# Performance work log

Hardware: AMD Instinct MI355X
Metric: run time of the kernel (lower is better)

The kernel has to match this reference:

```python
import jax, jax.numpy as jnp
import numpy as np

L, H, DK, DV, D, DH, V, S, B = 2, 12, 64, 64, 768, 3072, 32000, 1024, 2


def _layernorm(x):
    # matches custom LayerNorm: mean over last dim, biased std, no eps, no affine
    mu = jnp.mean(x, axis=-1, keepdims=True)
    sigma = jnp.sqrt(jnp.mean(jnp.square(x - mu), axis=-1, keepdims=True))
    return (x - mu) / sigma


def setup_inputs() -> dict:
    key = jax.random.key(0)
    ks = jax.random.split(key, 12)
    n = lambda k, shp: (0.02 * jax.random.normal(k, shp, dtype=jnp.float32))
    return {
        "x": jax.random.randint(ks[0], (B, S), 0, V),
        "ignore": jax.random.randint(ks[1], (B, S), 0, 2).astype(jnp.int32),
        "emb": n(ks[2], (V, D)),
        "pos": n(ks[3], (S, D)),
        "Wq": n(ks[4], (L, H, D, DK)), "bq": jnp.zeros((L, H, DK), jnp.float32),
        "Wk": n(ks[5], (L, H, D, DK)), "bk": jnp.zeros((L, H, DK), jnp.float32),
        "Wv": n(ks[6], (L, H, D, DV)), "bv": jnp.zeros((L, H, DV), jnp.float32),
        "Wo": n(ks[7], (L, H * DV, D)), "bo": jnp.zeros((L, D), jnp.float32),
        "W1": n(ks[8], (L, D, DH)), "b1": jnp.zeros((L, DH), jnp.float32),
        "W2": n(ks[9], (L, DH, D)), "b2": jnp.zeros((L, D), jnp.float32),
        "Wout": n(ks[10], (D, V)), "bout": jnp.zeros((V,), jnp.float32),
    }


def reference(x, ignore, emb, pos, Wq, bq, Wk, bk, Wv, bv, Wo, bo, W1, b1, W2, b2, Wout, bout):
    b, s = x.shape
    ign0 = (ignore == 0)  # True = valid token
    # token emb + position emb zeroed on ignored positions (dropout = eval/identity)
    h = emb[x] + pos[None, :, :] * ign0[:, :, None].astype(emb.dtype)

    # mask[b,i,j]: attend iff j<=i AND (ignore[j]==0 OR i==j)  (diagonal always kept)
    causal = jnp.tril(jnp.ones((s, s), dtype=bool))
    eye = jnp.eye(s, dtype=bool)
    allow = (ign0[:, None, None, :] | eye[None, None, :, :]) & causal[None, None, :, :]  # [b,1,i,j]

    scale = jnp.sqrt(jnp.asarray(DK, h.dtype))
    for l in range(L):
        q = jnp.einsum('bsd,hdk->bhsk', h, Wq[l]) + bq[l][None, :, None, :]
        k = jnp.einsum('bsd,hdk->bhsk', h, Wk[l]) + bk[l][None, :, None, :]
        v = jnp.einsum('bsd,hdv->bhsv', h, Wv[l]) + bv[l][None, :, None, :]
        scores = jnp.einsum('bhik,bhjk->bhij', q, k) / scale
        scores = jnp.where(allow, scores, -jnp.inf)
        p = jax.nn.softmax(scores, axis=-1)
        sa = jnp.einsum('bhij,bhjv->bhiv', p, v)
        sa = sa.transpose(0, 2, 1, 3).reshape(b, s, H * DV)  # concat heads (head-major order matches torch cat)
        attn_out = sa @ Wo[l] + bo[l]
        z = _layernorm(h + attn_out)
        # NOTE: original FeedForwardLayer applies GELU AFTER linear2 (faithful to source)
        f = jax.nn.gelu((z @ W1[l] + b1[l]) @ W2[l] + b2[l], approximate=False)
        h = _layernorm(z + f)
    return h @ Wout + bout
```

## Files before the change

### kernel.cpp

```cpp
#include <hip/hip_runtime.h>
#include <math.h>

static constexpr int L_ = 2, H_ = 12, D_ = 768, DH_ = 3072, V_ = 32000,
                     S_ = 1024, B_ = 2;
static constexpr int M_ = B_ * S_;

typedef __attribute__((ext_vector_type(4))) float f32x4;
typedef __attribute__((ext_vector_type(8))) short s16x8;
typedef __attribute__((ext_vector_type(2))) unsigned int u32x2;
typedef __attribute__((ext_vector_type(4))) unsigned int u32x4;

__device__ __forceinline__ unsigned short f2bf(float f) {
    unsigned u = __builtin_bit_cast(unsigned, f);
    u = (u + 0x7FFFu + ((u >> 16) & 1u)) >> 16;
    return (unsigned short)u;
}
__device__ __forceinline__ unsigned pack2(float a, float b) {
    return (unsigned)f2bf(a) | ((unsigned)f2bf(b) << 16);
}

__device__ __forceinline__ void gld16(const void* g, void* l) {
    __builtin_amdgcn_global_load_lds(
        (const __attribute__((address_space(1))) unsigned int*)g,
        (__attribute__((address_space(3))) unsigned int*)l, 16, 0, 0);
}

__global__ __launch_bounds__(256) void wtr_kernel(
    const float* __restrict__ in, unsigned short* __restrict__ out, int K, int N)
{
    __shared__ unsigned short t[64 * 68];
    const size_t mo = (size_t)blockIdx.z * K * N;
    in  += mo; out += mo;
    const int n0 = blockIdx.x * 64, k0 = blockIdx.y * 64;
    const int tid = threadIdx.x;
    const int kr = tid >> 2, nc = (tid & 3) * 16;
    const float* src = in + (size_t)(k0 + kr) * N + n0 + nc;
    #pragma unroll
    for (int j = 0; j < 4; ++j) {
        const float4 v = *(const float4*)(src + j * 4);
        *(u32x2*)&t[kr * 68 + nc + j * 4] = (u32x2){pack2(v.x, v.y), pack2(v.z, v.w)};
    }
    __syncthreads();
    const int nr = tid >> 2, kc = (tid & 3) * 16;
    unsigned short v16[16];
    #pragma unroll
    for (int j = 0; j < 16; ++j) v16[j] = t[(kc + j) * 68 + nr];
    unsigned short* dst = out + (size_t)(n0 + nr) * K + k0 + kc;
    ((u32x4*)dst)[0] = *(u32x4*)&v16[0];
    ((u32x4*)dst)[1] = *(u32x4*)&v16[8];
}

__global__ __launch_bounds__(256) void wtr3_kernel(
    const float* __restrict__ Wq, const float* __restrict__ Wk,
    const float* __restrict__ Wv, unsigned short* __restrict__ oq,
    unsigned short* __restrict__ ok, unsigned short* __restrict__ ov)
{
    __shared__ unsigned short t[64 * 68];
    const int z = blockIdx.z;
    const int which = z / 24, zz = z - which * 24;
    const float* in = (which == 0) ? Wq : (which == 1) ? Wk : Wv;
    unsigned short* out = (which == 0) ? oq : (which == 1) ? ok : ov;
    const size_t mo = (size_t)zz * D_ * 64;
    in += mo; out += mo;
    const int k0 = blockIdx.y * 64;
    const int tid = threadIdx.x;
    const int kr = tid >> 2, nc = (tid & 3) * 16;
    const float* src = in + (size_t)(k0 + kr) * 64 + nc;
    #pragma unroll
    for (int j = 0; j < 4; ++j) {
        const float4 v = *(const float4*)(src + j * 4);
        *(u32x2*)&t[kr * 68 + nc + j * 4] = (u32x2){pack2(v.x, v.y), pack2(v.z, v.w)};
    }
    __syncthreads();
    const int nr = tid >> 2, kc = (tid & 3) * 16;
    unsigned short v16[16];
    #pragma unroll
    for (int j = 0; j < 16; ++j) v16[j] = t[(kc + j) * 68 + nr];
    unsigned short* dst = out + (size_t)nr * D_ + k0 + kc;
    ((u32x4*)dst)[0] = *(u32x4*)&v16[0];
    ((u32x4*)dst)[1] = *(u32x4*)&v16[8];
}

__device__ __forceinline__ void xcd_decode(int& bx, int& by) {
    const int gx = gridDim.x, gy = gridDim.y;
    const int nwg = gx * gy;
    const int flat = blockIdx.y * gx + blockIdx.x;
    const int s = (flat & 7) * (nwg >> 3) + (flat >> 3);
    bx = s / gy;
    by = s % gy;
}

__device__ __forceinline__ void bt64_body(
    const unsigned short* __restrict__ A, const unsigned short* __restrict__ BT,
    const float* __restrict__ bias, void* __restrict__ Cp,
    int N, int K, int act, int k0off, int klen, int bx, int by)
{
    __shared__ unsigned short AB[12288];
    unsigned short* As = AB;
    unsigned short* Bs = AB + 4096;
    const int tid = threadIdx.x;
    const int l = tid & 63, w = tid >> 6;
    const int lq = l & 15, lg = l >> 4;
    const int brow = by * 64, bn = bx * 128;

    f32x4 acc[4][2];
    #pragma unroll
    for (int i = 0; i < 4; ++i)
        #pragma unroll
        for (int j = 0; j < 2; ++j) acc[i][j] = (f32x4)0.f;

    const int arow = tid >> 3;
    const int aq   = (tid & 7) ^ (arow & 7);
    const unsigned short* Abase = A  + (size_t)(brow + arow) * K + k0off + aq * 8;
    const unsigned short* Bbase = BT + (size_t)(bn   + arow) * K + k0off + aq * 8;

    for (int k0 = 0; k0 < klen; k0 += 64) {
        #pragma unroll
        for (int r = 0; r < 2; ++r)
            gld16(Abase + (size_t)r * 32 * K + k0, (char*)As + r * 4096 + tid * 16);
        #pragma unroll
        for (int r = 0; r < 4; ++r)
            gld16(Bbase + (size_t)r * 32 * K + k0, (char*)Bs + r * 4096 + tid * 16);
        __syncthreads();

        #pragma unroll
        for (int kk = 0; kk < 2; ++kk) {
            s16x8 af[4], bf[2];
            #pragma unroll
            for (int mf = 0; mf < 4; ++mf) {
                const int row = mf * 16 + lq;
                const int gg  = (kk * 4 + lg) ^ (row & 7);
                af[mf] = *(const s16x8*)((const char*)As + row * 128 + gg * 16);
            }
            #pragma unroll
            for (int nf = 0; nf < 2; ++nf) {
                const int col = w * 32 + nf * 16 + lq;
                const int gg  = (kk * 4 + lg) ^ (col & 7);
                bf[nf] = *(const s16x8*)((const char*)Bs + col * 128 + gg * 16);
            }
            #pragma unroll
            for (int mf = 0; mf < 4; ++mf)
                #pragma unroll
                for (int nf = 0; nf < 2; ++nf)
                    acc[mf][nf] = __builtin_amdgcn_mfma_f32_16x16x32_bf16(
                        af[mf], bf[nf], acc[mf][nf], 0, 0, 0);
        }
        __syncthreads();
    }

    if (act == 3) {
        #pragma unroll
        for (int nf = 0; nf < 2; ++nf) {
            const int c = w * 32 + nf * 16 + lq;
            const float bb = bias[bn + c];
            #pragma unroll
            for (int mf = 0; mf < 4; ++mf) {
                const int srel = mf * 16 + lg * 4;
                u32x2 pk;
                pk[0] = pack2(acc[mf][nf][0] + bb, acc[mf][nf][1] + bb);
                pk[1] = pack2(acc[mf][nf][2] + bb, acc[mf][nf][3] + bb);
                const int byo = (c * 128 + srel * 2) ^ ((c & 7) << 4);
                *(u32x2*)((char*)AB + byo) = pk;
            }
        }
        __syncthreads();
        const int row = tid >> 1, half = tid & 1;
        const int gcf = bn + row;
        const int head = gcf >> 6, d = gcf & 63;
        const int b = brow >> 10;
        const int sb = (brow & (S_ - 1)) + half * 32;
        unsigned short* dst = (unsigned short*)Cp +
            (((size_t)b * H_ + head) * 64 + d) * S_ + sb;
        #pragma unroll
        for (int u = 0; u < 4; ++u) {
            const int byo = (row * 128 + half * 64 + u * 16) ^ ((row & 7) << 4);
            ((u32x4*)dst)[u] = *(const u32x4*)((const char*)AB + byo);
        }
        return;
    }
    #pragma unroll
    for (int nf = 0; nf < 2; ++nf) {
        const int gcol = bn + w * 32 + nf * 16 + lq;
        const float bb = (act == 4) ? 0.f : bias[gcol];
        #pragma unroll
        for (int mf = 0; mf < 4; ++mf)
            #pragma unroll
            for (int rg = 0; rg < 4; ++rg) {
                const int grow = brow + mf * 16 + lg * 4 + rg;
                float vv = acc[mf][nf][rg] + bb;
                if (act == 1) vv = 0.5f * vv * (1.0f + erff(vv * 0.70710678118654752f));
                if (act == 2)
                    ((unsigned short*)Cp)[(size_t)grow * N + gcol] = f2bf(vv);
                else
                    ((float*)Cp)[(size_t)grow * N + gcol] = vv;
            }
    }
}

__global__ __launch_bounds__(256) void gemm_bt64(
    const unsigned short* __restrict__ A, const unsigned short* __restrict__ BT,
    const float* __restrict__ bias, void* __restrict__ C, int N, int K, int act)
{
    int bx, by; xcd_decode(bx, by);
    bt64_body(A, BT, bias, C, N, K, act, 0, K, bx, by);
}

__global__ __launch_bounds__(256) void gemm_qkv64(
    const unsigned short* __restrict__ A,
    const unsigned short* __restrict__ qT, const unsigned short* __restrict__ kT,
    const unsigned short* __restrict__ vT,
    const float* __restrict__ bq, const float* __restrict__ bk, const float* __restrict__ bv,
    unsigned short* __restrict__ q, unsigned short* __restrict__ k,
    unsigned short* __restrict__ v)
{
    const unsigned short* BT; const float* bi; unsigned short* C; int act;
    if (blockIdx.z == 0)      { BT = qT; bi = bq; C = q; act = 2; }
    else if (blockIdx.z == 1) { BT = kT; bi = bk; C = k; act = 2; }
    else                      { BT = vT; bi = bv; C = v; act = 3; }
    int bx, by; xcd_decode(bx, by);
    bt64_body(A, BT, bi, C, 768, 768, act, 0, 768, bx, by);
}

__global__ __launch_bounds__(256) void gemm_w2sk(
    const unsigned short* __restrict__ A, const unsigned short* __restrict__ BT,
    const float* __restrict__ bias, float* __restrict__ C0, float* __restrict__ C1)
{
    int bx, by; xcd_decode(bx, by);
    if (blockIdx.z == 0)
        bt64_body(A, BT, bias, C0, 768, DH_, 0, 0, 1536, bx, by);
    else
        bt64_body(A, BT, bias, C1, 768, DH_, 4, 1536, 1536, bx, by);
}

__global__ __launch_bounds__(512) void gemm_deep(
    const unsigned short* __restrict__ A, const unsigned short* __restrict__ BT,
    const float* __restrict__ bias, float* __restrict__ C, int N, int K)
{
    __shared__ char lds[131072];
    const int tid = threadIdx.x;
    const int l = tid & 63, w = tid >> 6;
    const int wr = w >> 2, wc = w & 3;
    const int lq = l & 15, lg = l >> 4;

    int bx, by;
    {
        const int gx = gridDim.x, gy = gridDim.y;
        const int nwg = gx * gy;
        const int flat = blockIdx.y * gx + blockIdx.x;
        const int s = (flat & 7) * (nwg >> 3) + (flat >> 3);
        bx = s / gy; by = s % gy;
    }
    const int brow = by * 256, bn = bx * 256;
    const int NT = K >> 6;

    const int srow = (w << 3) + (l >> 3);
    const int sgr  = (l & 7) ^ (l >> 3);
    const size_t soff = (size_t)srow * K + sgr * 8;
    const unsigned short* Ag = A  + (size_t)brow * K + soff;
    const unsigned short* Bg = BT + (size_t)bn   * K + soff;
    const size_t r64  = (size_t)64 * K;
    const size_t r128 = (size_t)128 * K;
    char* const dA = lds + w * 1024;
    char* const dB = lds + 65536 + w * 1024;

#define STG_A(CB, HF, KT) do {                                                   \
    gld16(Ag + (size_t)(HF) * r128 + (size_t)(KT) * 64,                          \
          dA + (CB) * 32768 + (HF) * 16384);                                     \
    gld16(Ag + (size_t)(HF) * r128 + r64 + (size_t)(KT) * 64,                    \
          dA + (CB) * 32768 + (HF) * 16384 + 8192); } while (0)
#define STG_B(CB, HF, KT) do {                                                   \
    gld16(Bg + (size_t)(HF) * r128 + (size_t)(KT) * 64,                          \
          dB + (CB) * 32768 + (HF) * 16384);                                     \
    gld16(Bg + (size_t)(HF) * r128 + r64 + (size_t)(KT) * 64,                    \
          dB + (CB) * 32768 + (HF) * 16384 + 8192); } while (0)

    f32x4 acc[8][4];
    #pragma unroll
    for (int i = 0; i < 8; ++i)
        #pragma unroll
        for (int j = 0; j < 4; ++j) acc[i][j] = (f32x4)0.f;

    STG_A(0, 0, 0); STG_A(0, 1, 0); STG_B(0, 0, 0); STG_B(0, 1, 0);
    STG_A(1, 0, 1); STG_B(1, 0, 1);
    asm volatile("s_waitcnt vmcnt(4)" ::: "memory");
    __builtin_amdgcn_s_barrier();

    for (int t = 0; t < NT; ++t) {
        const int c = t & 1;
        const char* Ab = lds + c * 32768;
        const char* Bb = lds + 65536 + c * 32768;
        s16x8 af[4], bf[4];

        #pragma unroll
        for (int mf = 0; mf < 4; ++mf) {
            const int row = wr * 128 + mf * 16 + lq;
            af[mf] = *(const s16x8*)(Ab + row * 128 + ((lg ^ (row & 7)) << 4));
        }
        #pragma unroll
        for (int nf = 0; nf < 4; ++nf) {
            const int col = wc * 64 + nf * 16 + lq;
            bf[nf] = *(const s16x8*)(Bb + col * 128 + ((lg ^ (col & 7)) << 4));
        }
        if (t + 1 < NT) STG_A(c ^ 1, 1, t + 1);
        asm volatile("s_waitcnt lgkmcnt(0)" ::: "memory");
        __builtin_amdgcn_sched_barrier(0);
        __builtin_amdgcn_s_barrier();
        __builtin_amdgcn_s_setprio(1);
        #pragma unroll
        for (int mf = 0; mf < 4; ++mf)
            #pragma unroll
            for (int nf = 0; nf < 4; ++nf)
                acc[mf][nf] = __builtin_amdgcn_mfma_f32_16x16x32_bf16(
                    af[mf], bf[nf], acc[mf][nf], 0, 0, 0);
        __builtin_amdgcn_s_setprio(0);
        __builtin_amdgcn_s_barrier();

        #pragma unroll
        for (int mf = 0; mf < 4; ++mf) {
            const int row = wr * 128 + (mf + 4) * 16 + lq;
            af[mf] = *(const s16x8*)(Ab + row * 128 + ((lg ^ (row & 7)) << 4));
        }
        if (t + 1 < NT) STG_B(c ^ 1, 1, t + 1);
        asm volatile("s_waitcnt lgkmcnt(0)" ::: "memory");
        __builtin_amdgcn_sched_barrier(0);
        __builtin_amdgcn_s_barrier();
        __builtin_amdgcn_s_setprio(1);
        #pragma unroll
        for (int mf = 0; mf < 4; ++mf)
            #pragma unroll
            for (int nf = 0; nf < 4; ++nf)
                acc[mf + 4][nf] = __builtin_amdgcn_mfma_f32_16x16x32_bf16(
                    af[mf], bf[nf], acc[mf + 4][nf], 0, 0, 0);
        __builtin_amdgcn_s_setprio(0);
        __builtin_amdgcn_s_barrier();

        #pragma unroll
        for (int mf = 0; mf < 4; ++mf) {
            const int row = wr * 128 + mf * 16 + lq;
            af[mf] = *(const s16x8*)(Ab + row * 128 + (((4 + lg) ^ (row & 7)) << 4));
        }
        #pragma unroll
        for (int nf = 0; nf < 4; ++nf) {
            const int col = wc * 64 + nf * 16 + lq;
            bf[nf] = *(const s16x8*)(Bb + col * 128 + (((4 + lg) ^ (col & 7)) << 4));
        }
        asm volatile("s_waitcnt lgkmcnt(0)" ::: "memory");
        __builtin_amdgcn_sched_barrier(0);
        __builtin_amdgcn_s_barrier();
        __builtin_amdgcn_s_setprio(1);
        #pragma unroll
        for (int mf = 0; mf < 4; ++mf)
            #pragma unroll
            for (int nf = 0; nf < 4; ++nf)
                acc[mf][nf] = __builtin_amdgcn_mfma_f32_16x16x32_bf16(
                    af[mf], bf[nf], acc[mf][nf], 0, 0, 0);
        __builtin_amdgcn_s_setprio(0);
        __builtin_amdgcn_s_barrier();

        #pragma unroll
        for (int mf = 0; mf < 4; ++mf) {
            const int row = wr * 128 + (mf + 4) * 16 + lq;
            af[mf] = *(const s16x8*)(Ab + row * 128 + (((4 + lg) ^ (row & 7)) << 4));
        }
        asm volatile("s_waitcnt lgkmcnt(0)" ::: "memory");
        __builtin_amdgcn_sched_barrier(0);
        __builtin_amdgcn_s_barrier();
        __builtin_amdgcn_s_setprio(1);
        #pragma unroll
        for (int mf = 0; mf < 4; ++mf)
            #pragma unroll
            for (int nf = 0; nf < 4; ++nf)
                acc[mf + 4][nf] = __builtin_amdgcn_mfma_f32_16x16x32_bf16(
                    af[mf], bf[nf], acc[mf + 4][nf], 0, 0, 0);
        __builtin_amdgcn_s_setprio(0);

        if (t + 2 < NT) {
            STG_A(c, 0, t + 2); STG_B(c, 0, t + 2);
            asm volatile("s_waitcnt vmcnt(4)" ::: "memory");
            __builtin_amdgcn_s_barrier();
        } else if (t + 1 < NT) {
            asm volatile("s_waitcnt vmcnt(0)" ::: "memory");
            __builtin_amdgcn_s_barrier();
        }
    }
#undef STG_A
#undef STG_B

    #pragma unroll
    for (int nf = 0; nf < 4; ++nf) {
        const int gcol = bn + wc * 64 + nf * 16 + lq;
        const float bb = bias[gcol];
        #pragma unroll
        for (int mf = 0; mf < 8; ++mf)
            #pragma unroll
            for (int rg = 0; rg < 4; ++rg) {
                const int grow = brow + wr * 128 + mf * 16 + lg * 4 + rg;
                C[(size_t)grow * N + gcol] = acc[mf][nf][rg] + bb;
            }
    }
}

__global__ __launch_bounds__(256) void gemm_f32b(
    const unsigned short* __restrict__ A, const float* __restrict__ B,
    const float* __restrict__ bias, float* __restrict__ C, int N, int K)
{
    __shared__ unsigned short As[8192];
    __shared__ unsigned short Bs[8192];
    const int tid = threadIdx.x;
    const int l   = tid & 63, wid = tid >> 6;
    const int wr  = wid >> 1, wc = wid & 1;
    const int brow = blockIdx.y * 128, bn = blockIdx.x * 128;
    f32x4 acc[4][4];
    #pragma unroll
    for (int i = 0; i < 4; ++i)
        #pragma unroll
        for (int j = 0; j < 4; ++j) acc[i][j] = (f32x4)0.f;
    const int arow = tid >> 3;
    const int aq   = (tid & 7) ^ (arow & 7);
    const int bkq  = tid >> 5, bnq = tid & 31;
    for (int k0 = 0; k0 < K; k0 += 64) {
        #pragma unroll
        for (int r = 0; r < 4; ++r)
            gld16(A + (size_t)(brow + r * 32 + arow) * K + k0 + aq * 8,
                  (char*)As + r * 4096 + wid * 1024);
        #pragma unroll
        for (int r = 0; r < 2; ++r) {
            const int kb = r * 32 + bkq * 4;
            const float* pp = B + (size_t)(k0 + kb) * N + bn + bnq * 4;
            const float4 v0 = *(const float4*)(pp);
            const float4 v1 = *(const float4*)(pp + N);
            const float4 v2 = *(const float4*)(pp + 2 * (size_t)N);
            const float4 v3 = *(const float4*)(pp + 3 * (size_t)N);
            const int g = kb >> 3, bytek = (kb & 4) * 2;
            const float* f0 = (const float*)&v0; const float* f1 = (const float*)&v1;
            const float* f2 = (const float*)&v2; const float* f3 = (const float*)&v3;
            #pragma unroll
            for (int i = 0; i < 4; ++i) {
                const int n = bnq * 4 + i;
                char* dst = (char*)Bs + n * 128 + ((g ^ (n & 7)) * 16) + bytek;
                *(u32x2*)dst = (u32x2){pack2(f0[i], f1[i]), pack2(f2[i], f3[i])};
            }
        }
        __syncthreads();
        #pragma unroll
        for (int kk = 0; kk < 2; ++kk) {
            s16x8 af[4], bf[4];
            #pragma unroll
            for (int mf = 0; mf < 4; ++mf) {
                const int row = wr * 64 + mf * 16 + (l & 15);
                const int gg  = (kk * 4 + (l >> 4)) ^ (row & 7);
                af[mf] = *(const s16x8*)((const char*)As + row * 128 + gg * 16);
            }
            #pragma unroll
            for (int nf = 0; nf < 4; ++nf) {
                const int col = wc * 64 + nf * 16 + (l & 15);
                const int gg  = (kk * 4 + (l >> 4)) ^ (col & 7);
                bf[nf] = *(const s16x8*)((const char*)Bs + col * 128 + gg * 16);
            }
            #pragma unroll
            for (int mf = 0; mf < 4; ++mf)
                #pragma unroll
                for (int nf = 0; nf < 4; ++nf)
                    acc[mf][nf] = __builtin_amdgcn_mfma_f32_16x16x32_bf16(
                        af[mf], bf[nf], acc[mf][nf], 0, 0, 0);
        }
        __syncthreads();
    }
    const int lr = l >> 4, lc = l & 15;
    #pragma unroll
    for (int nf = 0; nf < 4; ++nf) {
        const int gcol = bn + wc * 64 + nf * 16 + lc;
        const float bb = bias[gcol];
        #pragma unroll
        for (int mf = 0; mf < 4; ++mf)
            #pragma unroll
            for (int rg = 0; rg < 4; ++rg) {
                const int grow = brow + wr * 64 + mf * 16 + lr * 4 + rg;
                C[(size_t)grow * N + gcol] = acc[mf][nf][rg] + bb;
            }
    }
}

__global__ __launch_bounds__(256) void fattn_kernel(
    const unsigned short* __restrict__ qm, const unsigned short* __restrict__ km,
    const unsigned short* __restrict__ vt, const int* __restrict__ ign,
    unsigned short* __restrict__ sab)
{
    __shared__ unsigned short Ks[2][4096];
    __shared__ unsigned short VTs[2][4096];
    __shared__ float addvs[2][64];
    __shared__ unsigned short PTs[4][1024];

    const int hh = blockIdx.y, b = blockIdx.z;
    const int zy = b * 12 + hh;
    const int qt = (zy >= 16) ? (15 - blockIdx.x) : blockIdx.x;

    const int tid = threadIdx.x;
    const int l = tid & 63, w = tid >> 6;
    const int g = l >> 4, lq = l & 15;
    const int i = qt * 64 + w * 16 + lq;

    const size_t qgb = ((size_t)(b * S_ + i)) * D_ + hh * 64;
    const s16x8 qf0 = *(const s16x8*)(qm + qgb + g * 8);
    const s16x8 qf1 = *(const s16x8*)(qm + qgb + 32 + g * 8);

    f32x4 accO[4];
    #pragma unroll
    for (int d = 0; d < 4; ++d) accO[d] = (f32x4)0.f;
    float mrun = -1e30f, lrun = 0.f;

    const int srow = tid >> 3, sg = tid & 7;
    const size_t kbase = (size_t)(b * S_) * D_ + hh * 64;
    const size_t vbase = ((size_t)(b * H_ + hh) * 64) * S_;

    auto stage = [&](int t, int bufi) {
        const int j0 = t * 64;
        #pragma unroll
        for (int r = 0; r < 2; ++r) {
            const int row = r * 32 + srow;
            const int gsw = (sg ^ (row & 7)) * 8;
            gld16(km + kbase + (size_t)(j0 + row) * D_ + gsw,
                  (char*)&Ks[bufi][0] + (r * 256 + tid) * 16);
            gld16(vt + vbase + (size_t)row * S_ + j0 + gsw,
                  (char*)&VTs[bufi][0] + (r * 256 + tid) * 16);
        }
        if (tid < 64)
            addvs[bufi][tid] = (ign[b * S_ + j0 + tid] == 0) ? 0.f : -INFINITY;
    };

    stage(0, 0);
    asm volatile("s_waitcnt vmcnt(0) lgkmcnt(0)" ::: "memory");
    __syncthreads();

    for (int t = 0; t <= qt; ++t) {
        const int cur = t & 1;
        const int j0 = t * 64;
        if (t < qt) stage(t + 1, cur ^ 1);

        f32x4 adv[4];
        #pragma unroll
        for (int kf = 0; kf < 4; ++kf)
            adv[kf] = *(const f32x4*)&addvs[cur][kf * 16 + g * 4];

        f32x4 sacc[4];
        #pragma unroll
        for (int kf = 0; kf < 4; ++kf) sacc[kf] = (f32x4)0.f;
        __builtin_amdgcn_s_setprio(1);
        #pragma unroll
        for (int kk = 0; kk < 2; ++kk) {
            const s16x8 qv = kk ? qf1 : qf0;
            #pragma unroll
            for (int kf = 0; kf < 4; ++kf) {
                const int row = kf * 16 + lq;
                const s16x8 kv = *(const s16x8*)((const char*)&Ks[cur][0] + row * 128 +
                                                 (((kk * 4 + g) ^ (row & 7)) * 16));
                sacc[kf] = __builtin_amdgcn_mfma_f32_16x16x32_bf16(kv, qv, sacc[kf], 0, 0, 0);
            }
        }
        __builtin_amdgcn_s_setprio(0);

        float tmax = -INFINITY;
        if (t < qt) {
            #pragma unroll
            for (int kf = 0; kf < 4; ++kf)
                #pragma unroll
                for (int rg = 0; rg < 4; ++rg) {
                    const float s = fmaf(sacc[kf][rg], 0.125f, adv[kf][rg]);
                    sacc[kf][rg] = s;
                    tmax = fmaxf(tmax, s);
                }
        } else {
            #pragma unroll
            for (int kf = 0; kf < 4; ++kf)
                #pragma unroll
                for (int rg = 0; rg < 4; ++rg) {
                    const int j = j0 + kf * 16 + g * 4 + rg;
                    const float sv = sacc[kf][rg] * 0.125f;
                    const float s = (j > i) ? -INFINITY
                                  : (j == i ? sv : sv + adv[kf][rg]);
                    sacc[kf][rg] = s;
                    tmax = fmaxf(tmax, s);
                }
        }
        tmax = fmaxf(tmax, __shfl_xor(tmax, 16));
        tmax = fmaxf(tmax, __shfl_xor(tmax, 32));
        const float mnew = fmaxf(mrun, tmax);
        const float fac = __expf(mrun - mnew);
        float psum = 0.f;
        #pragma unroll
        for (int kf = 0; kf < 4; ++kf)
            #pragma unroll
            for (int rg = 0; rg < 4; ++rg) {
                const float p = __expf(sacc[kf][rg] - mnew);
                sacc[kf][rg] = p;
                psum += p;
            }
        psum += __shfl_xor(psum, 16);
        psum += __shfl_xor(psum, 32);
        lrun = lrun * fac + psum;
        mrun = mnew;
        #pragma unroll
        for (int d = 0; d < 4; ++d) accO[d] *= fac;

        char* ptw = (char*)&PTs[w][0];
        #pragma unroll
        for (int kf = 0; kf < 4; ++kf) {
            u32x2 pk;
            pk[0] = pack2(sacc[kf][0], sacc[kf][1]);
            pk[1] = pack2(sacc[kf][2], sacc[kf][3]);
            *(u32x2*)(ptw + lq * 128 +
                      (((kf * 2 + (g >> 1)) ^ (lq & 7)) * 16) + (g & 1) * 8) = pk;
        }
        __builtin_amdgcn_s_setprio(1);
        #pragma unroll
        for (int kh = 0; kh < 2; ++kh) {
            const s16x8 pb = *(const s16x8*)(ptw + lq * 128 +
                                             (((kh * 4 + g) ^ (lq & 7)) * 16));
            #pragma unroll
            for (int df = 0; df < 4; ++df) {
                const int row = df * 16 + lq;
                const s16x8 vf = *(const s16x8*)((const char*)&VTs[cur][0] + row * 128 +
                                                 (((kh * 4 + g) ^ (row & 7)) * 16));
                accO[df] = __builtin_amdgcn_mfma_f32_16x16x32_bf16(vf, pb, accO[df], 0, 0, 0);
            }
        }
        __builtin_amdgcn_s_setprio(0);
        asm volatile("s_waitcnt vmcnt(0)" ::: "memory");
        __syncthreads();
    }

    const float inv = 1.0f / lrun;
    unsigned short* orow = sab + ((size_t)(b * S_ + i)) * D_ + hh * 64;
    #pragma unroll
    for (int df = 0; df < 4; ++df) {
        u32x2 pk;
        pk[0] = pack2(accO[df][0] * inv, accO[df][1] * inv);
        pk[1] = pack2(accO[df][2] * inv, accO[df][3] * inv);
        *(u32x2*)(orow + df * 16 + g * 4) = pk;
    }
}

__global__ __launch_bounds__(256) void embed_kernel(
    const int* __restrict__ x, const int* __restrict__ ign,
    const float* __restrict__ emb, const float* __restrict__ pos,
    float* __restrict__ h, unsigned short* __restrict__ hbf)
{
    const int row = blockIdx.x;
    const int s = row & (S_ - 1);
    const int tok = x[row];
    const float keep = (ign[row] == 0) ? 1.0f : 0.0f;
    const float* er = emb + (size_t)tok * D_;
    const float* pr = pos + (size_t)s * D_;
    float* hr = h + (size_t)row * D_;
    unsigned short* hb = hbf + (size_t)row * D_;
    for (int d = threadIdx.x; d < D_; d += 256) {
        const float t = er[d] + pr[d] * keep;
        hr[d] = t;
        hb[d] = f2bf(t);
    }
}

__global__ __launch_bounds__(256) void add_ln_kernel(
    const float* __restrict__ X, const float* __restrict__ Y0,
    const float* __restrict__ Y1, float* __restrict__ out,
    unsigned short* __restrict__ outbf, int mode)
{
    const int row = blockIdx.x * 4 + (threadIdx.x >> 6);
    const int l = threadIdx.x & 63;
    const float4* xr = (const float4*)(X + (size_t)row * D_);
    const float4* y0 = (const float4*)(Y0 + (size_t)row * D_);
    const float4* y1 = (const float4*)(Y1 + (size_t)row * D_);
    float4 t[3];
    float s0 = 0.f;
    #pragma unroll
    for (int k = 0; k < 3; ++k) {
        const float4 a = xr[k * 64 + l];
        float4 b = y0[k * 64 + l];
        if (mode == 1) {
            const float4 c = y1[k * 64 + l];
            b.x += c.x; b.y += c.y; b.z += c.z; b.w += c.w;
            b.x = 0.5f * b.x * (1.0f + erff(b.x * 0.70710678118654752f));
            b.y = 0.5f * b.y * (1.0f + erff(b.y * 0.70710678118654752f));
            b.z = 0.5f * b.z * (1.0f + erff(b.z * 0.70710678118654752f));
            b.w = 0.5f * b.w * (1.0f + erff(b.w * 0.70710678118654752f));
        }
        t[k].x = a.x + b.x; t[k].y = a.y + b.y;
        t[k].z = a.z + b.z; t[k].w = a.w + b.w;
        s0 += t[k].x + t[k].y + t[k].z + t[k].w;
    }
    #pragma unroll
    for (int o = 32; o; o >>= 1) s0 += __shfl_xor(s0, o);
    const float mu = s0 * (1.0f / D_);
    float s1 = 0.f;
    #pragma unroll
    for (int k = 0; k < 3; ++k) {
        t[k].x -= mu; t[k].y -= mu; t[k].z -= mu; t[k].w -= mu;
        s1 += t[k].x * t[k].x + t[k].y * t[k].y + t[k].z * t[k].z + t[k].w * t[k].w;
    }
    #pragma unroll
    for (int o = 32; o; o >>= 1) s1 += __shfl_xor(s1, o);
    const float inv = 1.0f / sqrtf(s1 * (1.0f / D_));
    float4* orow = (float4*)(out + (size_t)row * D_);
    u32x2* obf = (u32x2*)(outbf + (size_t)row * D_);
    #pragma unroll
    for (int k = 0; k < 3; ++k) {
        float4 r;
        r.x = t[k].x * inv; r.y = t[k].y * inv;
        r.z = t[k].z * inv; r.w = t[k].w * inv;
        orow[k * 64 + l] = r;
        u32x2 pk; pk[0] = pack2(r.x, r.y); pk[1] = pack2(r.z, r.w);
        obf[k * 64 + l] = pk;
    }
}

extern "C" void kernel_launch(void* const* d_in, const int* in_sizes, int n_in,
                              void* d_out, int out_size, void* d_ws, size_t ws_size,
                              hipStream_t stream)
{
    const int*   x    = (const int*)d_in[0];
    const int*   ign  = (const int*)d_in[1];
    const float* emb  = (const float*)d_in[2];
    const float* pos  = (const float*)d_in[3];
    const float* Wq   = (const float*)d_in[4];
    const float* bq   = (const float*)d_in[5];
    const float* Wk   = (const float*)d_in[6];
    const float* bk   = (const float*)d_in[7];
    const float* Wv   = (const float*)d_in[8];
    const float* bv   = (const float*)d_in[9];
    const float* Wo   = (const float*)d_in[10];
    const float* bo   = (const float*)d_in[11];
    const float* W1   = (const float*)d_in[12];
    const float* b1   = (const float*)d_in[13];
    const float* W2   = (const float*)d_in[14];
    const float* b2   = (const float*)d_in[15];
    const float* Wout = (const float*)d_in[16];
    const float* bout = (const float*)d_in[17];
    float* outp = (float*)d_out;

    const size_t RC = (size_t)M_ * D_;
    const size_t F1 = (size_t)M_ * DH_;
    const size_t WH = (size_t)H_ * 64 * D_;
    const size_t WF = (size_t)D_ * DH_;
    const size_t WOUTE = (size_t)V_ * D_;

    char* wsp = (char*)d_ws;
    size_t wsleft = ws_size;
    char* dop = (char*)d_out;
    auto alloc = [&](size_t bytes, bool must_ws) -> void* {
        bytes = (bytes + 255) & ~(size_t)255;
        if (wsleft >= bytes) { void* p = wsp; wsp += bytes; wsleft -= bytes; return p; }
        if (must_ws) return nullptr;
        void* p = dop; dop += bytes; return p;
    };

    unsigned short* hbf   = (unsigned short*)alloc(RC * 2, true);
    unsigned short* woutT = (unsigned short*)alloc(WOUTE * 2, true);
    float* h    = (float*)alloc(RC * 4, false);
    float* z    = (float*)alloc(RC * 4, false);
    float* tmp  = (float*)alloc(RC * 4, false);
    float* tmp1 = (float*)alloc(RC * 4, false);
    unsigned short* zbf   = (unsigned short*)alloc(RC * 2, false);
    unsigned short* sabbf = (unsigned short*)alloc(RC * 2, false);
    unsigned short* qbf   = (unsigned short*)alloc(RC * 2, false);
    unsigned short* kbf   = (unsigned short*)alloc(RC * 2, false);
    unsigned short* vtb   = (unsigned short*)alloc(RC * 2, false);
    unsigned short* f1bf  = (unsigned short*)alloc(F1 * 2, false);
    unsigned short* wqT = (unsigned short*)alloc(L_ * WH * 2, false);
    unsigned short* wkT = (unsigned short*)alloc(L_ * WH * 2, false);
    unsigned short* wvT = (unsigned short*)alloc(L_ * WH * 2, false);
    unsigned short* woT = (unsigned short*)alloc(L_ * WH * 2, false);
    unsigned short* w1T = (unsigned short*)alloc(L_ * WF * 2, false);
    unsigned short* w2T = (unsigned short*)alloc(L_ * WF * 2, false);

    embed_kernel<<<M_, 256, 0, stream>>>(x, ign, emb, pos, h, hbf);

    wtr3_kernel<<<dim3(1, 12, 72), 256, 0, stream>>>(Wq, Wk, Wv, wqT, wkT, wvT);
    wtr_kernel<<<dim3(12, 12, L_), 256, 0, stream>>>(Wo, woT, D_, D_);
    wtr_kernel<<<dim3(48, 12, L_), 256, 0, stream>>>(W1, w1T, D_, DH_);
    wtr_kernel<<<dim3(12, 48, L_), 256, 0, stream>>>(W2, w2T, DH_, D_);
    if (woutT)
        wtr_kernel<<<dim3(V_ / 64, 12, 1), 256, 0, stream>>>(Wout, woutT, D_, V_);

    for (int l = 0; l < L_; ++l) {
        gemm_qkv64<<<dim3(6, 32, 3), 256, 0, stream>>>(
            hbf, wqT + l * WH, wkT + l * WH, wvT + l * WH,
            bq + l * 768, bk + l * 768, bv + l * 768, qbf, kbf, vtb);

        fattn_kernel<<<dim3(S_ / 64, H_, B_), 256, 0, stream>>>(
            qbf, kbf, vtb, ign, sabbf);

        gemm_bt64<<<dim3(6, 32), 256, 0, stream>>>(
            sabbf, woT + l * WH, bo + l * D_, tmp, D_, D_, 0);
        add_ln_kernel<<<M_ / 4, 256, 0, stream>>>(h, tmp, tmp, z, zbf, 0);

        gemm_bt64<<<dim3(24, 32), 256, 0, stream>>>(
            zbf, w1T + l * WF, b1 + l * DH_, f1bf, DH_, D_, 2);
        gemm_w2sk<<<dim3(6, 32, 2), 256, 0, stream>>>(
            f1bf, w2T + l * WF, b2 + l * D_, tmp, tmp1);
        add_ln_kernel<<<M_ / 4, 256, 0, stream>>>(z, tmp, tmp1, h, hbf, 1);
    }

    if (woutT)
        gemm_deep<<<dim3(V_ / 256, M_ / 256), 512, 0, stream>>>(
            hbf, woutT, bout, outp, V_, D_);
    else
        gemm_f32b<<<dim3(V_ / 128, M_ / 128), 256, 0, stream>>>(
            hbf, Wout, bout, outp, V_, D_);
}
```

Baseline: 451.4 us.

## Shrink vocab GEMM tiles to 128x128 and split-K the Wo projection

The output-vocabulary GEMM moves from 256x256 tiles with 128KB LDS to 128x128 tiles with 64KB LDS and a simpler double-buffered pipeline, declaring launch bounds that allow more resident blocks. This gives more workgroups and occupancy per CU, at the cost of less data reuse per tile. The Wo projection GEMM is split along K into two halves written to separate buffers, and the add+layernorm kernel gains a mode that sums them without GELU. This doubles the block count of a small GEMM to fill more CUs, in exchange for extra partial-sum memory traffic.

```diff
diff --git a/kernel.cpp b/kernel.cpp
--- a/kernel.cpp
+++ b/kernel.cpp
@@ -232,11 +232,22 @@
         bt64_body(A, BT, bias, C1, 768, DH_, 4, 1536, 1536, bx, by);
 }
 
-__global__ __launch_bounds__(512) void gemm_deep(
+__global__ __launch_bounds__(256) void gemm_wosk(
+    const unsigned short* __restrict__ A, const unsigned short* __restrict__ BT,
+    const float* __restrict__ bias, float* __restrict__ C0, float* __restrict__ C1)
+{
+    int bx, by; xcd_decode(bx, by);
+    if (blockIdx.z == 0)
+        bt64_body(A, BT, bias, C0, 768, 768, 0, 0, 384, bx, by);
+    else
+        bt64_body(A, BT, bias, C1, 768, 768, 4, 384, 384, bx, by);
+}
+
+__global__ __launch_bounds__(512, 4) void gemm_deep2(
     const unsigned short* __restrict__ A, const unsigned short* __restrict__ BT,
     const float* __restrict__ bias, float* __restrict__ C, int N, int K)
 {
-    __shared__ char lds[131072];
+    __shared__ char lds[65536];
     const int tid = threadIdx.x;
     const int l = tid & 63, w = tid >> 6;
     const int wr = w >> 2, wc = w & 3;
@@ -250,7 +261,7 @@
         const int s = (flat & 7) * (nwg >> 3) + (flat >> 3);
         bx = s / gy; by = s % gy;
     }
-    const int brow = by * 256, bn = bx * 256;
+    const int brow = by * 128, bn = bx * 128;
     const int NT = K >> 6;
 
     const int srow = (w << 3) + (l >> 3);
@@ -258,50 +269,44 @@
     const size_t soff = (size_t)srow * K + sgr * 8;
     const unsigned short* Ag = A  + (size_t)brow * K + soff;
     const unsigned short* Bg = BT + (size_t)bn   * K + soff;
-    const size_t r64  = (size_t)64 * K;
-    const size_t r128 = (size_t)128 * K;
-    char* const dA = lds + w * 1024;
-    char* const dB = lds + 65536 + w * 1024;
-
-#define STG_A(CB, HF, KT) do {                                                   \
-    gld16(Ag + (size_t)(HF) * r128 + (size_t)(KT) * 64,                          \
-          dA + (CB) * 32768 + (HF) * 16384);                                     \
-    gld16(Ag + (size_t)(HF) * r128 + r64 + (size_t)(KT) * 64,                    \
-          dA + (CB) * 32768 + (HF) * 16384 + 8192); } while (0)
-#define STG_B(CB, HF, KT) do {                                                   \
-    gld16(Bg + (size_t)(HF) * r128 + (size_t)(KT) * 64,                          \
-          dB + (CB) * 32768 + (HF) * 16384);                                     \
-    gld16(Bg + (size_t)(HF) * r128 + r64 + (size_t)(KT) * 64,                    \
-          dB + (CB) * 32768 + (HF) * 16384 + 8192); } while (0)
-
-    f32x4 acc[8][4];
-    #pragma unroll
-    for (int i = 0; i < 8; ++i)
-        #pragma unroll
-        for (int j = 0; j < 4; ++j) acc[i][j] = (f32x4)0.f;
-
-    STG_A(0, 0, 0); STG_A(0, 1, 0); STG_B(0, 0, 0); STG_B(0, 1, 0);
-    STG_A(1, 0, 1); STG_B(1, 0, 1);
-    asm volatile("s_waitcnt vmcnt(4)" ::: "memory");
+    const size_t r64 = (size_t)64 * K;
+
+#define STG_A2(CB, KT) do {                                                      \
+    gld16(Ag + (size_t)(KT) * 64, lds + (CB) * 16384 + w * 1024);                \
+    gld16(Ag + r64 + (size_t)(KT) * 64,                                          \
+          lds + (CB) * 16384 + 8192 + w * 1024); } while (0)
+#define STG_B2(CB, KT) do {                                                      \
+    gld16(Bg + (size_t)(KT) * 64, lds + 32768 + (CB) * 16384 + w * 1024);        \
+    gld16(Bg + r64 + (size_t)(KT) * 64,                                          \
+          lds + 32768 + (CB) * 16384 + 8192 + w * 1024); } while (0)
+
+    f32x4 acc[4][2];
+    #pragma unroll
+    for (int i = 0; i < 4; ++i)
+        #pragma unroll
+        for (int j = 0; j < 2; ++j) acc[i][j] = (f32x4)0.f;
+
+    STG_A2(0, 0); STG_B2(0, 0);
+    asm volatile("s_waitcnt vmcnt(0)" ::: "memory");
     __builtin_amdgcn_s_barrier();
 
     for (int t = 0; t < NT; ++t) {
         const int c = t & 1;
-        const char* Ab = lds + c * 32768;
-        const char* Bb = lds + 65536 + c * 32768;
-        s16x8 af[4], bf[4];
+        const char* Ab = lds + c * 16384;
+        const char* Bb = lds + 32768 + c * 16384;
+        s16x8 af[4], bf[2];
 
         #pragma unroll
         for (int mf = 0; mf < 4; ++mf) {
-            const int row = wr * 128 + mf * 16 + lq;
+            const int row = wr * 64 + mf * 16 + lq;
             af[mf] = *(const s16x8*)(Ab + row * 128 + ((lg ^ (row & 7)) << 4));
         }
         #pragma unroll
-        for (int nf = 0; nf < 4; ++nf) {
-            const int col = wc * 64 + nf * 16 + lq;
+        for (int nf = 0; nf < 2; ++nf) {
+            const int col = wc * 32 + nf * 16 + lq;
             bf[nf] = *(const s16x8*)(Bb + col * 128 + ((lg ^ (col & 7)) << 4));
         }
-        if (t + 1 < NT) STG_A(c ^ 1, 1, t + 1);
+        if (t + 1 < NT) STG_A2(c ^ 1, t + 1);
         asm volatile("s_waitcnt lgkmcnt(0)" ::: "memory");
         __builtin_amdgcn_sched_barrier(0);
         __builtin_amdgcn_s_barrier();
@@ -309,7 +314,7 @@
         #pragma unroll
         for (int mf = 0; mf < 4; ++mf)
             #pragma unroll
-            for (int nf = 0; nf < 4; ++nf)
+            for (int nf = 0; nf < 2; ++nf)
                 acc[mf][nf] = __builtin_amdgcn_mfma_f32_16x16x32_bf16(
                     af[mf], bf[nf], acc[mf][nf], 0, 0, 0);
         __builtin_amdgcn_s_setprio(0);
@@ -317,10 +322,15 @@
 
         #pragma unroll
         for (int mf = 0; mf < 4; ++mf) {
-            const int row = wr * 128 + (mf + 4) * 16 + lq;
-            af[mf] = *(const s16x8*)(Ab + row * 128 + ((lg ^ (row & 7)) << 4));
-        }
-        if (t + 1 < NT) STG_B(c ^ 1, 1, t + 1);
+            const int row = wr * 64 + mf * 16 + lq;
+            af[mf] = *(const s16x8*)(Ab + row * 128 + (((4 + lg) ^ (row & 7)) << 4));
+        }
+        #pragma unroll
+        for (int nf = 0; nf < 2; ++nf) {
+            const int col = wc * 32 + nf * 16 + lq;
+            bf[nf] = *(const s16x8*)(Bb + col * 128 + (((4 + lg) ^ (col & 7)) << 4));
+        }
+        if (t + 1 < NT) STG_B2(c ^ 1, t + 1);
         asm volatile("s_waitcnt lgkmcnt(0)" ::: "memory");
         __builtin_amdgcn_sched_barrier(0);
         __builtin_amdgcn_s_barrier();
@@ -328,73 +338,27 @@
         #pragma unroll
         for (int mf = 0; mf < 4; ++mf)
             #pragma unroll
-            for (int nf = 0; nf < 4; ++nf)
-                acc[mf + 4][nf] = __builtin_amdgcn_mfma_f32_16x16x32_bf16(
-                    af[mf], bf[nf], acc[mf + 4][nf], 0, 0, 0);
-        __builtin_amdgcn_s_setprio(0);
-        __builtin_amdgcn_s_barrier();
-
-        #pragma unroll
-        for (int mf = 0; mf < 4; ++mf) {
-            const int row = wr * 128 + mf * 16 + lq;
-            af[mf] = *(const s16x8*)(Ab + row * 128 + (((4 + lg) ^ (row & 7)) << 4));
-        }
-        #pragma unroll
-        for (int nf = 0; nf < 4; ++nf) {
-            const int col = wc * 64 + nf * 16 + lq;
-            bf[nf] = *(const s16x8*)(Bb + col * 128 + (((4 + lg) ^ (col & 7)) << 4));
-        }
-        asm volatile("s_waitcnt lgkmcnt(0)" ::: "memory");
-        __builtin_amdgcn_sched_barrier(0);
-        __builtin_amdgcn_s_barrier();
-        __builtin_amdgcn_s_setprio(1);
-        #pragma unroll
-        for (int mf = 0; mf < 4; ++mf)
-            #pragma unroll
-            for (int nf = 0; nf < 4; ++nf)
+            for (int nf = 0; nf < 2; ++nf)
                 acc[mf][nf] = __builtin_amdgcn_mfma_f32_16x16x32_bf16(
                     af[mf], bf[nf], acc[mf][nf], 0, 0, 0);
         __builtin_amdgcn_s_setprio(0);
+
+        if (t + 1 < NT)
+            asm volatile("s_waitcnt vmcnt(0)" ::: "memory");
         __builtin_amdgcn_s_barrier();
-
-        #pragma unroll
-        for (int mf = 0; mf < 4; ++mf) {
-            const int row = wr * 128 + (mf + 4) * 16 + lq;
-            af[mf] = *(const s16x8*)(Ab + row * 128 + (((4 + lg) ^ (row & 7)) << 4));
-        }
-        asm volatile("s_waitcnt lgkmcnt(0)" ::: "memory");
-        __builtin_amdgcn_sched_barrier(0);
-        __builtin_amdgcn_s_barrier();
-        __builtin_amdgcn_s_setprio(1);
+    }
+#undef STG_A2
+#undef STG_B2
+
+    #pragma unroll
+    for (int nf = 0; nf < 2; ++nf) {
+        const int gcol = bn + wc * 32 + nf * 16 + lq;
+        const float bb = bias[gcol];
         #pragma unroll
         for (int mf = 0; mf < 4; ++mf)
             #pragma unroll
-            for (int nf = 0; nf < 4; ++nf)
-                acc[mf + 4][nf] = __builtin_amdgcn_mfma_f32_16x16x32_bf16(
-                    af[mf], bf[nf], acc[mf + 4][nf], 0, 0, 0);
-        __builtin_amdgcn_s_setprio(0);
-
-        if (t + 2 < NT) {
-            STG_A(c, 0, t + 2); STG_B(c, 0, t + 2);
-            asm volatile("s_waitcnt vmcnt(4)" ::: "memory");
-            __builtin_amdgcn_s_barrier();
-        } else if (t + 1 < NT) {
-            asm volatile("s_waitcnt vmcnt(0)" ::: "memory");
-            __builtin_amdgcn_s_barrier();
-        }
-    }
-#undef STG_A
-#undef STG_B
-
-    #pragma unroll
-    for (int nf = 0; nf < 4; ++nf) {
-        const int gcol = bn + wc * 64 + nf * 16 + lq;
-        const float bb = bias[gcol];
-        #pragma unroll
-        for (int mf = 0; mf < 8; ++mf)
-            #pragma unroll
             for (int rg = 0; rg < 4; ++rg) {
-                const int grow = brow + wr * 128 + mf * 16 + lg * 4 + rg;
+                const int grow = brow + wr * 64 + mf * 16 + lg * 4 + rg;
                 C[(size_t)grow * N + gcol] = acc[mf][nf][rg] + bb;
             }
     }
@@ -676,9 +640,11 @@
     for (int k = 0; k < 3; ++k) {
         const float4 a = xr[k * 64 + l];
         float4 b = y0[k * 64 + l];
-        if (mode == 1) {
+        if (mode != 0) {
             const float4 c = y1[k * 64 + l];
             b.x += c.x; b.y += c.y; b.z += c.z; b.w += c.w;
+        }
+        if (mode == 1) {
             b.x = 0.5f * b.x * (1.0f + erff(b.x * 0.70710678118654752f));
             b.y = 0.5f * b.y * (1.0f + erff(b.y * 0.70710678118654752f));
             b.z = 0.5f * b.z * (1.0f + erff(b.z * 0.70710678118654752f));
@@ -789,9 +755,9 @@
         fattn_kernel<<<dim3(S_ / 64, H_, B_), 256, 0, stream>>>(
             qbf, kbf, vtb, ign, sabbf);
 
-        gemm_bt64<<<dim3(6, 32), 256, 0, stream>>>(
-            sabbf, woT + l * WH, bo + l * D_, tmp, D_, D_, 0);
-        add_ln_kernel<<<M_ / 4, 256, 0, stream>>>(h, tmp, tmp, z, zbf, 0);
+        gemm_wosk<<<dim3(6, 32, 2), 256, 0, stream>>>(
+            sabbf, woT + l * WH, bo + l * D_, tmp, tmp1);
+        add_ln_kernel<<<M_ / 4, 256, 0, stream>>>(h, tmp, tmp1, z, zbf, 2);
 
         gemm_bt64<<<dim3(24, 32), 256, 0, stream>>>(
             zbf, w1T + l * WF, b1 + l * DH_, f1bf, DH_, D_, 2);
@@ -801,7 +767,7 @@
     }
 
     if (woutT)
-        gemm_deep<<<dim3(V_ / 256, M_ / 256), 512, 0, stream>>>(
+        gemm_deep2<<<dim3(V_ / 128, M_ / 128), 512, 0, stream>>>(
             hbf, woutT, bout, outp, V_, D_);
     else
         gemm_f32b<<<dim3(V_ / 128, M_ / 128), 256, 0, stream>>>(
```

After: 456.3 us. Within noise of the previous version (+1.1%).

## Split QKV and Wo GEMMs for more workgroups; add split-K for Wo; cap deep GEMM occupancy

Applied to the files above, without the earlier changes.

Replaces the fused QKV GEMM with a dedicated 64x64-tile Q/K kernel, launched with twice as many column blocks, plus a separate V GEMM. The attention output projection is split along K into two halves, and the partial sums are combined inside add_ln with a new mode. The goal is more workgroups on the GPU's many CUs for these small GEMMs. The cost is extra kernel launches, an additional fp32 partial buffer read in layernorm, and a launch_bounds hint on the output GEMM that may change register allocation.

```diff
diff --git a/kernel.cpp b/kernel.cpp
--- a/kernel.cpp
+++ b/kernel.cpp
@@ -205,20 +205,80 @@
     bt64_body(A, BT, bias, C, N, K, act, 0, K, bx, by);
 }
 
-__global__ __launch_bounds__(256) void gemm_qkv64(
+__global__ __launch_bounds__(256) void gemm_qk64n(
     const unsigned short* __restrict__ A,
     const unsigned short* __restrict__ qT, const unsigned short* __restrict__ kT,
-    const unsigned short* __restrict__ vT,
-    const float* __restrict__ bq, const float* __restrict__ bk, const float* __restrict__ bv,
-    unsigned short* __restrict__ q, unsigned short* __restrict__ k,
-    unsigned short* __restrict__ v)
-{
-    const unsigned short* BT; const float* bi; unsigned short* C; int act;
-    if (blockIdx.z == 0)      { BT = qT; bi = bq; C = q; act = 2; }
-    else if (blockIdx.z == 1) { BT = kT; bi = bk; C = k; act = 2; }
-    else                      { BT = vT; bi = bv; C = v; act = 3; }
+    const float* __restrict__ bq, const float* __restrict__ bk,
+    unsigned short* __restrict__ q, unsigned short* __restrict__ k)
+{
+    __shared__ unsigned short As[4096];
+    __shared__ unsigned short Bs[4096];
+    const unsigned short* BT = (blockIdx.z == 0) ? qT : kT;
+    const float* bias = (blockIdx.z == 0) ? bq : bk;
+    unsigned short* C = (blockIdx.z == 0) ? q : k;
+    const int tid = threadIdx.x;
+    const int l = tid & 63, w = tid >> 6;
+    const int lq = l & 15, lg = l >> 4;
     int bx, by; xcd_decode(bx, by);
-    bt64_body(A, BT, bi, C, 768, 768, act, 0, 768, bx, by);
+    const int brow = by * 64, bn = bx * 64;
+    const int K = 768;
+
+    f32x4 acc[4];
+    #pragma unroll
+    for (int i = 0; i < 4; ++i) acc[i] = (f32x4)0.f;
+
+    const int arow = tid >> 3;
+    const int aq   = (tid & 7) ^ (arow & 7);
+    const unsigned short* Abase = A  + (size_t)(brow + arow) * K + aq * 8;
+    const unsigned short* Bbase = BT + (size_t)(bn   + arow) * K + aq * 8;
+
+    for (int k0 = 0; k0 < K; k0 += 64) {
+        #pragma unroll
+        for (int r = 0; r < 2; ++r) {
+            gld16(Abase + (size_t)r * 32 * K + k0, (char*)As + r * 4096 + tid * 16);
+            gld16(Bbase + (size_t)r * 32 * K + k0, (char*)Bs + r * 4096 + tid * 16);
+        }
+        __syncthreads();
+
+        #pragma unroll
+        for (int kk = 0; kk < 2; ++kk) {
+            s16x8 af[4], bf;
+            #pragma unroll
+            for (int mf = 0; mf < 4; ++mf) {
+                const int row = mf * 16 + lq;
+                const int gg  = (kk * 4 + lg) ^ (row & 7);
+                af[mf] = *(const s16x8*)((const char*)As + row * 128 + gg * 16);
+            }
+            {
+                const int col = w * 16 + lq;
+                const int gg  = (kk * 4 + lg) ^ (col & 7);
+                bf = *(const s16x8*)((const char*)Bs + col * 128 + gg * 16);
+            }
+            #pragma unroll
+            for (int mf = 0; mf < 4; ++mf)
+                acc[mf] = __builtin_amdgcn_mfma_f32_16x16x32_bf16(
+                    af[mf], bf, acc[mf], 0, 0, 0);
+        }
+        __syncthreads();
+    }
+
+    const int gcol = bn + w * 16 + lq;
+    const float bb = bias[gcol];
+    #pragma unroll
+    for (int mf = 0; mf < 4; ++mf)
+        #pragma unroll
+        for (int rg = 0; rg < 4; ++rg) {
+            const int grow = brow + mf * 16 + lg * 4 + rg;
+            C[(size_t)grow * 768 + gcol] = f2bf(acc[mf][rg] + bb);
+        }
+}
+
+__global__ __launch_bounds__(256) void gemm_v64(
+    const unsigned short* __restrict__ A, const unsigned short* __restrict__ vT,
+    const float* __restrict__ bv, unsigned short* __restrict__ v)
+{
+    int bx, by; xcd_decode(bx, by);
+    bt64_body(A, vT, bv, v, 768, 768, 3, 0, 768, bx, by);
 }
 
 __global__ __launch_bounds__(256) void gemm_w2sk(
@@ -232,7 +292,18 @@
         bt64_body(A, BT, bias, C1, 768, DH_, 4, 1536, 1536, bx, by);
 }
 
-__global__ __launch_bounds__(512) void gemm_deep(
+__global__ __launch_bounds__(256) void gemm_wosk(
+    const unsigned short* __restrict__ A, const unsigned short* __restrict__ BT,
+    const float* __restrict__ bias, float* __restrict__ C0, float* __restrict__ C1)
+{
+    int bx, by; xcd_decode(bx, by);
+    if (blockIdx.z == 0)
+        bt64_body(A, BT, bias, C0, 768, 768, 0, 0, 384, bx, by);
+    else
+        bt64_body(A, BT, bias, C1, 768, 768, 4, 384, 384, bx, by);
+}
+
+__global__ __launch_bounds__(512, 2) void gemm_deep(
     const unsigned short* __restrict__ A, const unsigned short* __restrict__ BT,
     const float* __restrict__ bias, float* __restrict__ C, int N, int K)
 {
@@ -676,9 +747,11 @@
     for (int k = 0; k < 3; ++k) {
         const float4 a = xr[k * 64 + l];
         float4 b = y0[k * 64 + l];
-        if (mode == 1) {
+        if (mode != 0) {
             const float4 c = y1[k * 64 + l];
             b.x += c.x; b.y += c.y; b.z += c.z; b.w += c.w;
+        }
+        if (mode == 1) {
             b.x = 0.5f * b.x * (1.0f + erff(b.x * 0.70710678118654752f));
             b.y = 0.5f * b.y * (1.0f + erff(b.y * 0.70710678118654752f));
             b.z = 0.5f * b.z * (1.0f + erff(b.z * 0.70710678118654752f));
@@ -782,16 +855,17 @@
         wtr_kernel<<<dim3(V_ / 64, 12, 1), 256, 0, stream>>>(Wout, woutT, D_, V_);
 
     for (int l = 0; l < L_; ++l) {
-        gemm_qkv64<<<dim3(6, 32, 3), 256, 0, stream>>>(
-            hbf, wqT + l * WH, wkT + l * WH, wvT + l * WH,
-            bq + l * 768, bk + l * 768, bv + l * 768, qbf, kbf, vtb);
+        gemm_qk64n<<<dim3(12, 32, 2), 256, 0, stream>>>(
+            hbf, wqT + l * WH, wkT + l * WH, bq + l * 768, bk + l * 768, qbf, kbf);
+        gemm_v64<<<dim3(6, 32), 256, 0, stream>>>(
+            hbf, wvT + l * WH, bv + l * 768, vtb);
 
         fattn_kernel<<<dim3(S_ / 64, H_, B_), 256, 0, stream>>>(
             qbf, kbf, vtb, ign, sabbf);
 
-        gemm_bt64<<<dim3(6, 32), 256, 0, stream>>>(
-            sabbf, woT + l * WH, bo + l * D_, tmp, D_, D_, 0);
-        add_ln_kernel<<<M_ / 4, 256, 0, stream>>>(h, tmp, tmp, z, zbf, 0);
+        gemm_wosk<<<dim3(6, 32, 2), 256, 0, stream>>>(
+            sabbf, woT + l * WH, bo + l * D_, tmp, tmp1);
+        add_ln_kernel<<<M_ / 4, 256, 0, stream>>>(h, tmp, tmp1, z, zbf, 2);
 
         gemm_bt64<<<dim3(24, 32), 256, 0, stream>>>(
             zbf, w1T + l * WF, b1 + l * DH_, f1bf, DH_, D_, 2);
```

New measurement: 468.8 us. 3.8% more time.
